# Performance work log

Hardware: AMD Instinct MI355X
Metric: run time of the kernel (lower is better)

## Reference

```python
import jax, jax.numpy as jnp
import numpy as np

N_QUBITS = 24
N_BLOCKS = 4


def _apply_ry(state, theta, q):
    # RY(theta) = [[cos(t/2), -sin(t/2)], [sin(t/2), cos(t/2)]] applied on qubit axis q
    half = theta * 0.5
    c, s = jnp.cos(half), jnp.sin(half)
    mat = jnp.stack([jnp.stack([c, -s]), jnp.stack([s, c])])  # [2,2]
    out = jnp.tensordot(mat, state, axes=([1], [q]))  # contracted axis moves to front
    return jnp.moveaxis(out, 0, q)


def _apply_cnot(state, ctrl, tgt):
    # Flip target axis on the control=1 slice.
    s = jnp.moveaxis(state, (ctrl, tgt), (0, 1))
    s = jnp.stack([s[0], jnp.flip(s[1], axis=0)])
    return jnp.moveaxis(s, (0, 1), (ctrl, tgt))


def setup_inputs() -> dict:
    key = jax.random.key(0)
    angles = jax.random.normal(key, (N_BLOCKS, N_QUBITS), dtype=jnp.float32)
    return {"angles": angles, "n_qubits": N_QUBITS, "n_blocks": N_BLOCKS}


def reference(angles, n_qubits, n_blocks):
    # |0...0> initial state. RY and CNOT are real matrices, so starting from a
    # real |0..0> state the amplitudes stay real; |psi|^2 == psi**2.
    state = jnp.zeros((2,) * n_qubits, dtype=angles.dtype)
    state = state.at[(0,) * n_qubits].set(1.0)
    for b in range(n_blocks):
        for q in range(n_qubits):
            state = _apply_ry(state, angles[b, q], q)
        for q in range(n_qubits - 1):
            state = _apply_cnot(state, q, q + 1)
    probs = jnp.square(state.reshape(-1))  # (2**n_qubits,)
    return probs
```

## Files before the change

kernel.cpp:

```cpp
#include <hip/hip_runtime.h>
#include <math.h>

#define N_QUBITS 24
#define N_BLOCKS 4
#define NSTATE (1 << N_QUBITS)


template <int CTRL>
__device__ __forceinline__ float dpp_mov(float v) {
    return __int_as_float(__builtin_amdgcn_update_dpp(
        __float_as_int(v), __float_as_int(v), CTRL, 0xF, 0xF, false));
}
template <int MASK>
__device__ __forceinline__ float xor_lanes(float v, int lane) {
    if constexpr (MASK == 1)       return dpp_mov<0xB1>(v);
    else if constexpr (MASK == 2)  return dpp_mov<0x4E>(v);
    else if constexpr (MASK == 4) {
        float lo = dpp_mov<0x114>(v);
        float hi = dpp_mov<0x104>(v);
        return (lane & 4) ? lo : hi;
    }
    else if constexpr (MASK == 8)  return dpp_mov<0x128>(v);
    else                           return __shfl_xor(v, MASK);
}

template <int B>
__device__ __forceinline__ void pair_bit32(float (&a)[32], float s, float c, int swap) {
#pragma unroll
    for (int g = 0; g < 16; ++g) {
        int r0 = ((g >> B) << (B + 1)) | (g & ((1 << B) - 1));
        int r1 = r0 | (1 << B);
        float v0 = a[r0], v1 = a[r1];
        float o0 = c * v0 - s * v1;
        float o1 = s * v0 + c * v1;
        a[r0] = swap ? o1 : o0;
        a[r1] = swap ? o0 : o1;
    }
}
template <int BT>
__device__ __forceinline__ void quad_gate32(float (&a)[32], float s, float c) {
#pragma unroll
    for (int g = 0; g < 8; ++g) {
        int lo  = g & ((1 << BT) - 1);
        int r00 = ((g >> BT) << (BT + 2)) | lo;
        int r01 = r00 | (1 << BT);
        int r10 = r00 | (2 << BT);
        int r11 = r00 | (3 << BT);
        float v00 = a[r00], v01 = a[r01], v10 = a[r10], v11 = a[r11];
        a[r00] = c * v00 - s * v01;
        a[r01] = s * v00 + c * v01;
        a[r10] = s * v10 + c * v11;
        a[r11] = c * v10 - s * v11;
    }
}
template <int MASK>
__device__ __forceinline__ void lane_gate32(float (&a)[32], float s, float c, int lane) {
    const int tau = (lane & MASK) ? 1 : 0;
    const int gam = (lane & (MASK << 1)) ? 1 : 0;
    const float A = gam ? (tau ? -s : s) : c;
    const float B = gam ? c : (tau ? s : -s);
#pragma unroll
    for (int r = 0; r < 32; ++r) {
        float p = xor_lanes<MASK>(a[r], lane);
        a[r] = A * a[r] + B * p;
    }
}
template <int MASK>
__device__ __forceinline__ void lane_gate32_regctrl(float (&a)[32], float s, float c,
                                                    int lane, int tau) {
    const float A0 = c,            B0 = tau ? s : -s;
    const float A1 = tau ? -s : s, B1 = c;
#pragma unroll
    for (int r = 0; r < 32; ++r) {
        float p = xor_lanes<MASK>(a[r], lane);
        float A = (r & 1) ? A1 : A0;
        float B = (r & 1) ? B1 : B0;
        a[r] = A * a[r] + B * p;
    }
}

__device__ __forceinline__ void p1_body(float (&a)[32], float* __restrict__ lds,
                                        float* __restrict__ dst, int blk,
                                        const float* __restrict__ scs,
                                        const float* __restrict__ scc,
                                        int lane, int w) {
    pair_bit32<4>(a, scs[0], scc[0], 0);
    quad_gate32<3>(a, scs[1], scc[1]);
    quad_gate32<2>(a, scs[2], scc[2]);
    quad_gate32<1>(a, scs[3], scc[3]);
    quad_gate32<0>(a, scs[4], scc[4]);

#pragma unroll
    for (int x = 0; x < 2; ++x) {
        __syncthreads();
#pragma unroll
        for (int j = 0; j < 16; ++j)
            lds[lane | (w << 6) | (j << 10)] = a[(x << 4) | j];
        __syncthreads();
#pragma unroll
        for (int m = 0; m < 16; ++m)
            a[(x << 4) | m] = lds[lane | (m << 6) | (w << 10)];
    }

    pair_bit32<3>(a, scs[5], scc[5], w & 1);
    quad_gate32<2>(a, scs[6], scc[6]);
    quad_gate32<1>(a, scs[7], scc[7]);
    quad_gate32<0>(a, scs[8], scc[8]);

    lane_gate32_regctrl<32>(a, scs[9], scc[9], lane, (lane >> 5) & 1);

#pragma unroll
    for (int k = 0; k < 32; ++k) {
        int G = ((lane >> 5) & 1) | ((k & 15) << 1) | (w << 5) | ((k >> 4) << 9);
        dst[((size_t)blk << 15) | (G << 5) | (size_t)(lane & 31)] = a[k];
    }
}

__global__ __launch_bounds__(1024, 2)
void pass1_pi_kernel(const float* __restrict__ src, float* __restrict__ dst,
                     const float* __restrict__ angles, int blk_b) {
    __shared__ float lds[16384];
    __shared__ float scs[10], scc[10];
    const int tid  = threadIdx.x;
    const int lane = tid & 63;
    const int w    = tid >> 6;
    const int blk  = blockIdx.x;
    const float* ang = angles + blk_b * N_QUBITS;

    if (tid < 10) {
        float s, c;
        sincosf(0.5f * ang[tid], &s, &c);
        scs[tid] = s; scc[tid] = c;
    }

    float a[32];
#pragma unroll
    for (int r = 0; r < 32; ++r)
        a[r] = src[((size_t)r << 19) | ((size_t)w << 15) | ((size_t)(lane >> 5) << 14)
                   | ((size_t)blk << 5) | (size_t)(lane & 31)];
    __syncthreads();

    p1_body(a, lds, dst, blk, scs, scc, lane, w);
}

__global__ __launch_bounds__(1024, 2)
void fused_init_p1_kernel(float* __restrict__ dst, const float* __restrict__ angles) {
    __shared__ float lds[16384];
    __shared__ float s0[24], c0[24];
    __shared__ float s1[10], c1[10];
    const int tid  = threadIdx.x;
    const int lane = tid & 63;
    const int w    = tid >> 6;
    const int blk  = blockIdx.x;

    if (tid < 24) {
        float s, c;
        sincosf(0.5f * angles[tid], &s, &c);
        s0[tid] = s; c0[tid] = c;
    } else if (tid >= 32 && tid < 42) {
        float s, c;
        sincosf(0.5f * angles[N_QUBITS + (tid - 32)], &s, &c);
        s1[tid - 32] = s; c1[tid - 32] = c;
    }

    float* f = lds;
    f[tid] = 0.0f;
    __syncthreads();
    if (tid == 0) f[0] = 1.0f;
    __syncthreads();
    if (tid < 512) {
        float s = s0[0], c = c0[0];
        float v0 = f[tid], v1 = f[tid | 512];
        f[tid]       = c * v0 - s * v1;
        f[tid | 512] = s * v0 + c * v1;
    }
    __syncthreads();
    for (int q = 1; q <= 9; ++q) {
        int bt = 9 - q;
        if (tid < 256) {
            float s = s0[q], c = c0[q];
            int lo  = tid & ((1 << bt) - 1);
            int r00 = ((tid >> bt) << (bt + 2)) | lo;
            int r01 = r00 | (1 << bt);
            int r10 = r00 | (2 << bt);
            int r11 = r00 | (3 << bt);
            float v00 = f[r00], v01 = f[r01], v10 = f[r10], v11 = f[r11];
            f[r00] = c * v00 - s * v01;
            f[r01] = s * v00 + c * v01;
            f[r10] = s * v10 + c * v11;
            f[r11] = c * v10 - s * v11;
        }
        __syncthreads();
    }

    float gval = 1.0f;
    {
        const int low = (blk << 5) | (lane & 31);
        int prev = (lane >> 5) & 1;
#pragma unroll
        for (int q = 10; q <= 23; ++q) {
            const int bt = 23 - q;
            const int b = (low >> bt) & 1;
            gval *= (b ^ prev) ? s0[q] : c0[q];
            prev = b;
        }
    }

    float a[32];
#pragma unroll
    for (int r = 0; r < 32; ++r)
        a[r] = f[(r << 5) | (w << 1) | (lane >> 5)] * gval;

    p1_body(a, lds, dst, blk, s1, c1, lane, w);
}

template <bool SQUARE>
__device__ __forceinline__ void p23_tail(float (&a)[32], float* __restrict__ lds,
                                         float* __restrict__ base,
                                         const float* __restrict__ scs,
                                         const float* __restrict__ scc,
                                         int lane, int w, int c14) {
    pair_bit32<4>(a, scs[0], scc[0], c14);
    quad_gate32<3>(a, scs[1], scc[1]);
    quad_gate32<2>(a, scs[2], scc[2]);
    quad_gate32<1>(a, scs[3], scc[3]);
    quad_gate32<0>(a, scs[4], scc[4]);

#pragma unroll
    for (int x = 0; x < 2; ++x) {
        if (x) __syncthreads();
#pragma unroll
        for (int j = 0; j < 16; ++j)
            lds[lane | (w << 6) | (j << 9)] = a[(x << 4) | j];
        __syncthreads();
#pragma unroll
        for (int m = 0; m < 16; ++m)
            a[(x << 4) | m] = lds[(lane & 31) | ((m & 1) << 5) | (((m >> 1) & 7) << 6)
                                  | ((lane >> 5) << 9) | (w << 10)];
    }

    pair_bit32<3>(a, scs[5], scc[5], (lane >> 5) & 1);
    quad_gate32<2>(a, scs[6], scc[6]);
    quad_gate32<1>(a, scs[7], scc[7]);
    quad_gate32<0>(a, scs[8], scc[8]);

    lane_gate32_regctrl<16>(a, scs[9], scc[9], lane, (lane >> 4) & 1);
    lane_gate32<8>(a, scs[10], scc[10], lane);
    lane_gate32<4>(a, scs[11], scc[11], lane);
    lane_gate32<2>(a, scs[12], scc[12], lane);
    lane_gate32<1>(a, scs[13], scc[13], lane);

    if (SQUARE) {
#pragma unroll
        for (int r = 0; r < 32; ++r) a[r] *= a[r];
    }

#pragma unroll
    for (int k = 0; k < 32; ++k)
        base[(lane & 31) | ((k & 15) << 5) | (((lane >> 5) & 1) << 9)
             | (w << 10) | (((k >> 4) & 1) << 13)] = a[k];
}

template <bool SQUARE>
__global__ __launch_bounds__(512, 4)
void pass23_pi_kernel(const float* __restrict__ src, float* __restrict__ dst,
                      const float* __restrict__ angles, int blk_b) {
    __shared__ float lds[8192];
    __shared__ float scs[14], scc[14];
    const int tid  = threadIdx.x;
    const int lane = tid & 63;
    const int w    = tid >> 6;
    const int chunk = blockIdx.x;
    float* __restrict__ base = dst + ((size_t)chunk << 14);
    const int c14 = chunk & 1;
    const float* ang = angles + blk_b * N_QUBITS;

    if (tid < 14) {
        float s, c;
        sincosf(0.5f * ang[10 + tid], &s, &c);
        scs[tid] = s; scc[tid] = c;
    }

    float a[32];
#pragma unroll
    for (int r = 0; r < 32; ++r)
        a[r] = src[((size_t)((r << 4) | (w << 1) | (lane >> 5)) << 15)
                   | ((size_t)chunk << 5) | (size_t)(lane & 31)];
    __syncthreads();

    p23_tail<SQUARE>(a, lds, base, scs, scc, lane, w, c14);
}

extern "C" void kernel_launch(void* const* d_in, const int* in_sizes, int n_in,
                              void* d_out, int out_size, void* d_ws, size_t ws_size,
                              hipStream_t stream) {
    const float* angles = (const float*)d_in[0];
    float* out = (float*)d_out;
    float* ws  = (float*)d_ws;

    fused_init_p1_kernel<<<512, 1024, 0, stream>>>(ws, angles);
    pass23_pi_kernel<false><<<1024, 512, 0, stream>>>(ws, out, angles, 1);

    pass1_pi_kernel<<<512, 1024, 0, stream>>>(out, ws, angles, 2);
    pass23_pi_kernel<false><<<1024, 512, 0, stream>>>(ws, out, angles, 2);

    pass1_pi_kernel<<<512, 1024, 0, stream>>>(out, ws, angles, 3);
    pass23_pi_kernel<true><<<1024, 512, 0, stream>>>(ws, out, angles, 3);
}
```

Measured before the change: 140.1 us.

## Regroup gate schedule into five passes instead of six

Repartitions the 96 RY gates and CNOT chains across five global-memory passes instead of six. Each pass applies more gates in registers and shared memory, using in-block transposes with XOR-swizzled layouts. The first kernel absorbs more of block 1 analytically. The goal is to cut one full read and write of the 64 MB state vector. The cost is more complex index permutations, extra LDS round trips per pass, and a higher risk of layout bugs.

```diff
diff --git a/kernel.cpp b/kernel.cpp
--- a/kernel.cpp
+++ b/kernel.cpp
@@ -53,6 +53,16 @@
         a[r11] = c * v10 - s * v11;
     }
 }
+__device__ __forceinline__ void pair_ctrl_reg0(float (&a)[32], float s, float c) {
+#pragma unroll
+    for (int g = 0; g < 16; ++g) {
+        float v0 = a[g], v1 = a[g | 16];
+        float o0 = c * v0 - s * v1;
+        float o1 = s * v0 + c * v1;
+        if (g & 1) { a[g] = o1; a[g | 16] = o0; }
+        else       { a[g] = o0; a[g | 16] = o1; }
+    }
+}
 template <int MASK>
 __device__ __forceinline__ void lane_gate32(float (&a)[32], float s, float c, int lane) {
     const int tau = (lane & MASK) ? 1 : 0;
@@ -66,6 +76,16 @@
     }
 }
 template <int MASK>
+__device__ __forceinline__ void lane_ry32(float (&a)[32], float s, float c, int lane) {
+    const int tau = (lane & MASK) ? 1 : 0;
+    const float A = c, B = tau ? s : -s;
+#pragma unroll
+    for (int r = 0; r < 32; ++r) {
+        float p = xor_lanes<MASK>(a[r], lane);
+        a[r] = A * a[r] + B * p;
+    }
+}
+template <int MASK>
 __device__ __forceinline__ void lane_gate32_regctrl(float (&a)[32], float s, float c,
                                                     int lane, int tau) {
     const float A0 = c,            B0 = tau ? s : -s;
@@ -79,87 +99,33 @@
     }
 }
 
-__device__ __forceinline__ void p1_body(float (&a)[32], float* __restrict__ lds,
-                                        float* __restrict__ dst, int blk,
-                                        const float* __restrict__ scs,
-                                        const float* __restrict__ scc,
-                                        int lane, int w) {
-    pair_bit32<4>(a, scs[0], scc[0], 0);
-    quad_gate32<3>(a, scs[1], scc[1]);
-    quad_gate32<2>(a, scs[2], scc[2]);
-    quad_gate32<1>(a, scs[3], scc[3]);
-    quad_gate32<0>(a, scs[4], scc[4]);
-
-#pragma unroll
-    for (int x = 0; x < 2; ++x) {
-        __syncthreads();
-#pragma unroll
-        for (int j = 0; j < 16; ++j)
-            lds[lane | (w << 6) | (j << 10)] = a[(x << 4) | j];
-        __syncthreads();
-#pragma unroll
-        for (int m = 0; m < 16; ++m)
-            a[(x << 4) | m] = lds[lane | (m << 6) | (w << 10)];
-    }
-
-    pair_bit32<3>(a, scs[5], scc[5], w & 1);
-    quad_gate32<2>(a, scs[6], scc[6]);
-    quad_gate32<1>(a, scs[7], scc[7]);
-    quad_gate32<0>(a, scs[8], scc[8]);
-
-    lane_gate32_regctrl<32>(a, scs[9], scc[9], lane, (lane >> 5) & 1);
-
-#pragma unroll
-    for (int k = 0; k < 32; ++k) {
-        int G = ((lane >> 5) & 1) | ((k & 15) << 1) | (w << 5) | ((k >> 4) << 9);
-        dst[((size_t)blk << 15) | (G << 5) | (size_t)(lane & 31)] = a[k];
-    }
-}
+#define IDT_TRANSPOSE(a, lds, lane, w)                                   \
+    _Pragma("unroll")                                                    \
+    for (int x = 0; x < 2; ++x) {                                        \
+        __syncthreads();                                                 \
+        _Pragma("unroll")                                                \
+        for (int j = 0; j < 16; ++j)                                     \
+            lds[(lane) | ((w) << 6) | (j << 10)] = a[(x << 4) | j];      \
+        __syncthreads();                                                 \
+        _Pragma("unroll")                                                \
+        for (int m = 0; m < 16; ++m)                                     \
+            a[(x << 4) | m] = lds[(lane) | (m << 6) | ((w) << 10)];      \
+    }
 
 __global__ __launch_bounds__(1024, 2)
-void pass1_pi_kernel(const float* __restrict__ src, float* __restrict__ dst,
-                     const float* __restrict__ angles, int blk_b) {
+void kernF(float* __restrict__ dst, const float* __restrict__ angles) {
     __shared__ float lds[16384];
-    __shared__ float scs[10], scc[10];
+    __shared__ float s0[24], c0[24], s1[15], c1[15];
     const int tid  = threadIdx.x;
     const int lane = tid & 63;
     const int w    = tid >> 6;
     const int blk  = blockIdx.x;
-    const float* ang = angles + blk_b * N_QUBITS;
-
-    if (tid < 10) {
-        float s, c;
-        sincosf(0.5f * ang[tid], &s, &c);
-        scs[tid] = s; scc[tid] = c;
-    }
-
-    float a[32];
-#pragma unroll
-    for (int r = 0; r < 32; ++r)
-        a[r] = src[((size_t)r << 19) | ((size_t)w << 15) | ((size_t)(lane >> 5) << 14)
-                   | ((size_t)blk << 5) | (size_t)(lane & 31)];
-    __syncthreads();
-
-    p1_body(a, lds, dst, blk, scs, scc, lane, w);
-}
-
-__global__ __launch_bounds__(1024, 2)
-void fused_init_p1_kernel(float* __restrict__ dst, const float* __restrict__ angles) {
-    __shared__ float lds[16384];
-    __shared__ float s0[24], c0[24];
-    __shared__ float s1[10], c1[10];
-    const int tid  = threadIdx.x;
-    const int lane = tid & 63;
-    const int w    = tid >> 6;
-    const int blk  = blockIdx.x;
 
     if (tid < 24) {
-        float s, c;
-        sincosf(0.5f * angles[tid], &s, &c);
+        float s, c; sincosf(0.5f * angles[tid], &s, &c);
         s0[tid] = s; c0[tid] = c;
-    } else if (tid >= 32 && tid < 42) {
-        float s, c;
-        sincosf(0.5f * angles[N_QUBITS + (tid - 32)], &s, &c);
+    } else if (tid >= 32 && tid < 47) {
+        float s, c; sincosf(0.5f * angles[24 + (tid - 32)], &s, &c);
         s1[tid - 32] = s; c1[tid - 32] = c;
     }
 
@@ -171,7 +137,7 @@
     if (tid < 512) {
         float s = s0[0], c = c0[0];
         float v0 = f[tid], v1 = f[tid | 512];
-        f[tid]       = c * v0 - s * v1;
+        f[tid] = c * v0 - s * v1;
         f[tid | 512] = s * v0 + c * v1;
     }
     __syncthreads();
@@ -193,102 +159,338 @@
         __syncthreads();
     }
 
-    float gval = 1.0f;
-    {
-        const int low = (blk << 5) | (lane & 31);
-        int prev = (lane >> 5) & 1;
-#pragma unroll
-        for (int q = 10; q <= 23; ++q) {
-            const int bt = 23 - q;
-            const int b = (low >> bt) & 1;
-            gval *= (b ^ prev) ? s0[q] : c0[q];
-            prev = b;
-        }
-    }
+    float gfix = 1.0f;
+#pragma unroll
+    for (int j = 0; j < 8; ++j) {
+        int x = ((blk >> j) ^ (blk >> (j + 1))) & 1;
+        gfix *= x ? s0[23 - j] : c0[23 - j];
+    }
+    const float fval = f[w | (lane << 4)];
+    const int b8 = (blk >> 8) & 1;
+    const int w0 = w & 1;
 
     float a[32];
 #pragma unroll
-    for (int r = 0; r < 32; ++r)
-        a[r] = f[(r << 5) | (w << 1) | (lane >> 5)] * gval;
-
-    p1_body(a, lds, dst, blk, s1, c1, lane, w);
-}
-
-template <bool SQUARE>
-__device__ __forceinline__ void p23_tail(float (&a)[32], float* __restrict__ lds,
-                                         float* __restrict__ base,
-                                         const float* __restrict__ scs,
-                                         const float* __restrict__ scc,
-                                         int lane, int w, int c14) {
-    pair_bit32<4>(a, scs[0], scc[0], c14);
+    for (int r = 0; r < 32; ++r) {
+        const int r0 = r & 1, r1 = (r >> 1) & 1, r2 = (r >> 2) & 1,
+                  r3 = (r >> 3) & 1, r4 = (r >> 4) & 1;
+        float g = gfix;
+        g *= (b8 ^ r0) ? s0[15] : c0[15];
+        g *= (r0 ^ r1) ? s0[14] : c0[14];
+        g *= (r1 ^ r2) ? s0[13] : c0[13];
+        g *= (r2 ^ r3) ? s0[12] : c0[12];
+        g *= (r3 ^ r4) ? s0[11] : c0[11];
+        g *= (r4 ^ w0) ? s0[10] : c0[10];
+        a[r] = fval * g;
+    }
+
+    lane_ry32<32>(a, s1[0], c1[0], lane);
+    lane_gate32<16>(a, s1[1], c1[1], lane);
+    lane_gate32<8>(a, s1[2], c1[2], lane);
+    lane_gate32<4>(a, s1[3], c1[3], lane);
+    lane_gate32<2>(a, s1[4], c1[4], lane);
+    lane_gate32<1>(a, s1[5], c1[5], lane);
+
+    IDT_TRANSPOSE(a, lds, lane, w)
+
+    pair_bit32<3>(a, s1[6], c1[6], lane & 1);
+    quad_gate32<2>(a, s1[7], c1[7]);
+    quad_gate32<1>(a, s1[8], c1[8]);
+    quad_gate32<0>(a, s1[9], c1[9]);
+    pair_ctrl_reg0(a, s1[10], c1[10]);
+
+    IDT_TRANSPOSE(a, lds, lane, w)
+
+    quad_gate32<3>(a, s1[11], c1[11]);
+    quad_gate32<2>(a, s1[12], c1[12]);
+    quad_gate32<1>(a, s1[13], c1[13]);
+    quad_gate32<0>(a, s1[14], c1[14]);
+
+#pragma unroll
+    for (int m = 0; m < 32; ++m)
+        dst[((size_t)blk << 15) | lane | (w << 6) | ((m & 15) << 10)
+            | ((m >> 4) << 14)] = a[m];
+}
+
+__global__ __launch_bounds__(1024, 2)
+void kernA(const float* __restrict__ src, float* __restrict__ dst,
+           const float* __restrict__ angles) {
+    __shared__ float lds[16384];
+    __shared__ float scs[15], scc[15];
+    const int tid  = threadIdx.x;
+    const int lane = tid & 63;
+    const int w    = tid >> 6;
+    const int blk  = blockIdx.x;
+
+    if (tid < 9) {
+        float s, c; sincosf(0.5f * angles[24 + 15 + tid], &s, &c);
+        scs[tid] = s; scc[tid] = c;
+    } else if (tid >= 16 && tid < 22) {
+        float s, c; sincosf(0.5f * angles[48 + (tid - 16)], &s, &c);
+        scs[9 + tid - 16] = s; scc[9 + tid - 16] = c;
+    }
+
+    float a[32];
+    const int hi4 = blk >> 5, lo4 = blk & 15, b13 = (blk >> 4) & 1;
+#pragma unroll
+    for (int r = 0; r < 32; ++r) {
+        int Fblk = ((r >> 4) & 1) | (w << 1) | ((r & 15) << 5);
+        a[r] = src[((size_t)Fblk << 15) | lane | (hi4 << 6) | (lo4 << 10)
+                   | (b13 << 14)];
+    }
+    __syncthreads();
+
+    pair_bit32<3>(a, scs[0], scc[0], blk & 1);
+    quad_gate32<2>(a, scs[1], scc[1]);
+    quad_gate32<1>(a, scs[2], scc[2]);
+    quad_gate32<0>(a, scs[3], scc[3]);
+
+    IDT_TRANSPOSE(a, lds, lane, w)
+
+    pair_bit32<3>(a, scs[4], scc[4], w & 1);
+    quad_gate32<2>(a, scs[5], scc[5]);
+    quad_gate32<1>(a, scs[6], scc[6]);
+    quad_gate32<0>(a, scs[7], scc[7]);
+    pair_ctrl_reg0(a, scs[8], scc[8]);
+
+    lane_ry32<32>(a, scs[9], scc[9], lane);
+    lane_gate32<16>(a, scs[10], scc[10], lane);
+    lane_gate32<8>(a, scs[11], scc[11], lane);
+    lane_gate32<4>(a, scs[12], scc[12], lane);
+    lane_gate32<2>(a, scs[13], scc[13], lane);
+    lane_gate32<1>(a, scs[14], scc[14], lane);
+
+#pragma unroll
+    for (int x = 0; x < 2; ++x) {
+        __syncthreads();
+#pragma unroll
+        for (int jj = 0; jj < 16; ++jj) {
+            int E37 = (jj >> 2) | ((w & 7) << 2);
+            int h = ((lane & 31) ^ E37) | (((lane >> 5) & 1) << 5)
+                  | (((w >> 3) & 1) << 6) | (E37 << 7)
+                  | ((jj & 1) << 12) | (((jj >> 1) & 1) << 13);
+            lds[h] = a[(x << 4) | jj];
+        }
+        __syncthreads();
+#pragma unroll
+        for (int mm = 0; mm < 16; ++mm) {
+            int E1822 = ((mm >> 2) & 1) | (((mm >> 3) & 1) << 1) | ((w & 7) << 2);
+            int h = (E1822 ^ (lane & 31)) | (((w >> 3) & 1) << 5)
+                  | (((lane >> 5) & 1) << 6) | ((lane & 31) << 7)
+                  | ((mm & 1) << 12) | (((mm >> 1) & 1) << 13);
+            float v = lds[h];
+            dst[((size_t)blk << 15) | lane | (x << 6) | ((mm & 1) << 7)
+                | (((mm >> 1) & 1) << 8) | (((mm >> 2) & 1) << 9)
+                | (((mm >> 3) & 1) << 10) | (w << 11)] = v;
+        }
+    }
+}
+
+__global__ __launch_bounds__(1024, 2)
+void kernB(const float* __restrict__ src, float* __restrict__ dst,
+           const float* __restrict__ angles) {
+    __shared__ float lds[16384];
+    __shared__ float scs[15], scc[15];
+    const int tid  = threadIdx.x;
+    const int lane = tid & 63;
+    const int w    = tid >> 6;
+    const int blk  = blockIdx.x;
+
+    if (tid < 15) {
+        float s, c; sincosf(0.5f * angles[48 + 6 + tid], &s, &c);
+        scs[tid] = s; scc[tid] = c;
+    }
+
+    float a[32];
+    const int fixedA = ((blk & 1) << 6) | (((blk >> 1) & 1) << 7)
+                     | (((blk >> 2) & 1) << 8) | (((blk >> 3) & 1) << 9)
+                     | (((blk >> 4) & 1) << 10) | ((blk >> 5) << 11);
+#pragma unroll
+    for (int r = 0; r < 32; ++r) {
+        int Ablk = w | (r << 4);
+        a[r] = src[((size_t)Ablk << 15) | lane | fixedA];
+    }
+    __syncthreads();
+
+    pair_bit32<4>(a, scs[0], scc[0], (blk >> 3) & 1);
     quad_gate32<3>(a, scs[1], scc[1]);
     quad_gate32<2>(a, scs[2], scc[2]);
     quad_gate32<1>(a, scs[3], scc[3]);
     quad_gate32<0>(a, scs[4], scc[4]);
 
-#pragma unroll
-    for (int x = 0; x < 2; ++x) {
-        if (x) __syncthreads();
-#pragma unroll
-        for (int j = 0; j < 16; ++j)
-            lds[lane | (w << 6) | (j << 9)] = a[(x << 4) | j];
-        __syncthreads();
-#pragma unroll
-        for (int m = 0; m < 16; ++m)
-            a[(x << 4) | m] = lds[(lane & 31) | ((m & 1) << 5) | (((m >> 1) & 7) << 6)
-                                  | ((lane >> 5) << 9) | (w << 10)];
-    }
-
-    pair_bit32<3>(a, scs[5], scc[5], (lane >> 5) & 1);
+    IDT_TRANSPOSE(a, lds, lane, w)
+
+    pair_bit32<3>(a, scs[5], scc[5], w & 1);
     quad_gate32<2>(a, scs[6], scc[6]);
     quad_gate32<1>(a, scs[7], scc[7]);
     quad_gate32<0>(a, scs[8], scc[8]);
-
-    lane_gate32_regctrl<16>(a, scs[9], scc[9], lane, (lane >> 4) & 1);
-    lane_gate32<8>(a, scs[10], scc[10], lane);
-    lane_gate32<4>(a, scs[11], scc[11], lane);
-    lane_gate32<2>(a, scs[12], scc[12], lane);
-    lane_gate32<1>(a, scs[13], scc[13], lane);
-
-    if (SQUARE) {
-#pragma unroll
-        for (int r = 0; r < 32; ++r) a[r] *= a[r];
-    }
-
-#pragma unroll
-    for (int k = 0; k < 32; ++k)
-        base[(lane & 31) | ((k & 15) << 5) | (((lane >> 5) & 1) << 9)
-             | (w << 10) | (((k >> 4) & 1) << 13)] = a[k];
-}
-
-template <bool SQUARE>
-__global__ __launch_bounds__(512, 4)
-void pass23_pi_kernel(const float* __restrict__ src, float* __restrict__ dst,
-                      const float* __restrict__ angles, int blk_b) {
-    __shared__ float lds[8192];
-    __shared__ float scs[14], scc[14];
+    lane_gate32_regctrl<32>(a, scs[9], scc[9], lane, (lane >> 5) & 1);
+    lane_gate32<16>(a, scs[10], scc[10], lane);
+    lane_gate32<8>(a, scs[11], scc[11], lane);
+    lane_gate32<4>(a, scs[12], scc[12], lane);
+    lane_gate32<2>(a, scs[13], scc[13], lane);
+    lane_gate32<1>(a, scs[14], scc[14], lane);
+
+#pragma unroll
+    for (int x = 0; x < 2; ++x) {
+        __syncthreads();
+#pragma unroll
+        for (int jj = 0; jj < 16; ++jj) {
+            int h = (lane & 7)
+                  | (((((lane >> 3) & 1)) ^ ((w >> 2) & 1)) << 3)
+                  | (((((lane >> 4) & 1)) ^ ((w >> 3) & 1)) << 4)
+                  | (((lane >> 5) & 1) << 5)
+                  | (((w >> 2) & 1) << 6) | (((w >> 3) & 1) << 7)
+                  | (((jj >> 3) & 1) << 8) | ((jj & 7) << 9)
+                  | ((w & 1) << 12) | (((w >> 1) & 1) << 13);
+            lds[h] = a[(jj << 1) | x];
+        }
+        __syncthreads();
+#pragma unroll
+        for (int mm = 0; mm < 16; ++mm) {
+            int h = (lane & 7)
+                  | ((((w & 1)) ^ ((lane >> 3) & 1)) << 3)
+                  | (((((w >> 1) & 1)) ^ ((lane >> 4) & 1)) << 4)
+                  | (((w >> 2) & 1) << 5)
+                  | (((lane >> 3) & 1) << 6) | (((lane >> 4) & 1) << 7)
+                  | (((lane >> 5) & 1) << 8) | ((mm & 7) << 9)
+                  | (((mm >> 3) & 1) << 12) | (((w >> 3) & 1) << 13);
+            float v = lds[h];
+            dst[((size_t)blk << 15) | lane | ((w & 7) << 6) | (x << 9)
+                | ((mm & 7) << 10) | (((mm >> 3) & 1) << 13)
+                | (((w >> 3) & 1) << 14)] = v;
+        }
+    }
+}
+
+__global__ __launch_bounds__(1024, 2)
+void kernC(const float* __restrict__ src, float* __restrict__ dst,
+           const float* __restrict__ angles) {
+    __shared__ float lds[16384];
+    __shared__ float scs[12], scc[12];
     const int tid  = threadIdx.x;
     const int lane = tid & 63;
     const int w    = tid >> 6;
-    const int chunk = blockIdx.x;
-    float* __restrict__ base = dst + ((size_t)chunk << 14);
-    const int c14 = chunk & 1;
-    const float* ang = angles + blk_b * N_QUBITS;
-
-    if (tid < 14) {
-        float s, c;
-        sincosf(0.5f * ang[10 + tid], &s, &c);
+    const int blk  = blockIdx.x;
+
+    if (tid < 3) {
+        float s, c; sincosf(0.5f * angles[48 + 21 + tid], &s, &c);
         scs[tid] = s; scc[tid] = c;
+    } else if (tid >= 8 && tid < 17) {
+        float s, c; sincosf(0.5f * angles[72 + (tid - 8)], &s, &c);
+        scs[3 + tid - 8] = s; scc[3 + tid - 8] = c;
     }
 
     float a[32];
-#pragma unroll
-    for (int r = 0; r < 32; ++r)
-        a[r] = src[((size_t)((r << 4) | (w << 1) | (lane >> 5)) << 15)
-                   | ((size_t)chunk << 5) | (size_t)(lane & 31)];
-    __syncthreads();
-
-    p23_tail<SQUARE>(a, lds, base, scs, scc, lane, w, c14);
+    const int fixedB = ((blk & 7) << 6) | (((blk >> 3) & 15) << 9)
+                     | (((blk >> 7) & 1) << 13) | (((blk >> 8) & 1) << 14);
+#pragma unroll
+    for (int r = 0; r < 32; ++r) {
+        int Bblk = (r & 31) | (w << 5);
+        a[r] = src[((size_t)Bblk << 15) | lane | fixedB];
+    }
+    __syncthreads();
+
+    pair_bit32<2>(a, scs[0], scc[0], lane & 1);
+    quad_gate32<1>(a, scs[1], scc[1]);
+    quad_gate32<0>(a, scs[2], scc[2]);
+
+    IDT_TRANSPOSE(a, lds, lane, w)
+
+    pair_bit32<3>(a, scs[3], scc[3], 0);
+    quad_gate32<2>(a, scs[4], scc[4]);
+    quad_gate32<1>(a, scs[5], scc[5]);
+    quad_gate32<0>(a, scs[6], scc[6]);
+    pair_ctrl_reg0(a, scs[7], scc[7]);
+
+#pragma unroll
+    for (int x = 0; x < 2; ++x) {
+        __syncthreads();
+#pragma unroll
+        for (int jj = 0; jj < 16; ++jj) {
+            int h = (lane & 7)
+                  | ((((lane >> 3) & 1) ^ (w & 1)) << 3)
+                  | ((((lane >> 4) & 1) ^ ((w >> 1) & 1)) << 4)
+                  | (((lane >> 5) & 1) << 5)
+                  | (((lane >> 3) & 1) << 6) | (((lane >> 4) & 1) << 7)
+                  | (((w >> 3) & 1) << 8) | (((w >> 2) & 1) << 9)
+                  | (jj << 10);
+            lds[h] = a[(x << 4) | jj];
+        }
+        __syncthreads();
+#pragma unroll
+        for (int mm = 0; mm < 16; ++mm) {
+            int h = ((lane >> 3) & 7)
+                  | (((mm & 1) ^ (lane & 1)) << 3)
+                  | ((((mm >> 1) & 1) ^ ((lane >> 1) & 1)) << 4)
+                  | (((mm >> 2) & 1) << 5)
+                  | ((mm & 1) << 6) | (((mm >> 1) & 1) << 7)
+                  | (((mm >> 3) & 1) << 8) | (((lane >> 2) & 1) << 9)
+                  | (w << 10);
+            a[(x << 4) | mm] = lds[h];
+        }
+    }
+
+    quad_gate32<3>(a, scs[8], scc[8]);
+    quad_gate32<2>(a, scs[9], scc[9]);
+    quad_gate32<1>(a, scs[10], scc[10]);
+    quad_gate32<0>(a, scs[11], scc[11]);
+
+#pragma unroll
+    for (int m = 0; m < 32; ++m)
+        dst[((size_t)blk << 15) | lane | ((m & 15) << 6) | ((m >> 4) << 10)
+            | (w << 11)] = a[m];
+}
+
+__global__ __launch_bounds__(1024, 2)
+void kernD(const float* __restrict__ src, float* __restrict__ dst,
+           const float* __restrict__ angles) {
+    __shared__ float lds[16384];
+    __shared__ float scs[15], scc[15];
+    const int tid  = threadIdx.x;
+    const int lane = tid & 63;
+    const int w    = tid >> 6;
+    const int blk  = blockIdx.x;
+
+    if (tid < 15) {
+        float s, c; sincosf(0.5f * angles[72 + 9 + tid], &s, &c);
+        scs[tid] = s; scc[tid] = c;
+    }
+
+    float a[32];
+#pragma unroll
+    for (int r = 0; r < 32; ++r) {
+        int Cblk = w | (r << 4);
+        a[r] = src[((size_t)Cblk << 15) | lane | (blk << 6)];
+    }
+    __syncthreads();
+
+    pair_bit32<4>(a, scs[0], scc[0], blk & 1);
+    quad_gate32<3>(a, scs[1], scc[1]);
+    quad_gate32<2>(a, scs[2], scc[2]);
+    quad_gate32<1>(a, scs[3], scc[3]);
+    quad_gate32<0>(a, scs[4], scc[4]);
+
+    IDT_TRANSPOSE(a, lds, lane, w)
+
+    pair_bit32<3>(a, scs[5], scc[5], w & 1);
+    quad_gate32<2>(a, scs[6], scc[6]);
+    quad_gate32<1>(a, scs[7], scc[7]);
+    quad_gate32<0>(a, scs[8], scc[8]);
+    lane_gate32_regctrl<32>(a, scs[9], scc[9], lane, (lane >> 5) & 1);
+    lane_gate32<16>(a, scs[10], scc[10], lane);
+    lane_gate32<8>(a, scs[11], scc[11], lane);
+    lane_gate32<4>(a, scs[12], scc[12], lane);
+    lane_gate32<2>(a, scs[13], scc[13], lane);
+    lane_gate32<1>(a, scs[14], scc[14], lane);
+
+#pragma unroll
+    for (int r = 0; r < 32; ++r) a[r] *= a[r];
+
+#pragma unroll
+    for (int m = 0; m < 32; ++m)
+        dst[((size_t)blk << 15) | ((m >> 4) << 14) | (w << 10) | ((m & 15) << 6)
+            | lane] = a[m];
 }
 
 extern "C" void kernel_launch(void* const* d_in, const int* in_sizes, int n_in,
@@ -298,12 +500,9 @@
     float* out = (float*)d_out;
     float* ws  = (float*)d_ws;
 
-    fused_init_p1_kernel<<<512, 1024, 0, stream>>>(ws, angles);
-    pass23_pi_kernel<false><<<1024, 512, 0, stream>>>(ws, out, angles, 1);
-
-    pass1_pi_kernel<<<512, 1024, 0, stream>>>(out, ws, angles, 2);
-    pass23_pi_kernel<false><<<1024, 512, 0, stream>>>(ws, out, angles, 2);
-
-    pass1_pi_kernel<<<512, 1024, 0, stream>>>(out, ws, angles, 3);
-    pass23_pi_kernel<true><<<1024, 512, 0, stream>>>(ws, out, angles, 3);
-}
+    kernF<<<512, 1024, 0, stream>>>(out, angles);
+    kernA<<<512, 1024, 0, stream>>>(out, ws, angles);
+    kernB<<<512, 1024, 0, stream>>>(ws, out, angles);
+    kernC<<<512, 1024, 0, stream>>>(out, ws, angles);
+    kernD<<<512, 1024, 0, stream>>>(ws, out, angles);
+}
```

After: 154.8 us. +10.5%, slower.
